# Optimization experiments

Hardware: AMD Instinct MI355X
Metric: run time of the kernel (lower is better)

Reference implementation:

```python
import jax, jax.numpy as jnp
import numpy as np

N = 50000

def gcn_conv(h, W, b, src, dst, n):
    # h: [N, Fin] -> linear transform then normalized scatter-add aggregation
    h = h @ W  # [N, Fout]
    # add self-loops (PyG GCNConv default)
    loop = jnp.arange(n, dtype=src.dtype)
    s = jnp.concatenate([src, loop])
    d = jnp.concatenate([dst, loop])
    # symmetric normalization: deg^{-1/2}[s] * deg^{-1/2}[d], deg over target index
    deg = jax.ops.segment_sum(jnp.ones_like(d, dtype=h.dtype), d, num_segments=n)
    dinv = jnp.where(deg > 0, jax.lax.rsqrt(deg), 0.0)
    norm = dinv[s] * dinv[d]  # [E+N]
    msg = h[s] * norm[:, None]  # gather + scale
    out = jax.ops.segment_sum(msg, d, num_segments=n)  # scatter-add
    return out + b


def setup_inputs() -> dict:
    key = jax.random.key(0)
    k1, k2, k3, k4, k5, k6 = jax.random.split(key, 6)
    Fin, Fh, Fout = 512, 256, 64
    E = 800000
    x = jax.random.normal(k1, (N, Fin), dtype=jnp.float32)
    edge_index = jax.random.randint(k2, (2, E), 0, N, dtype=jnp.int64)
    # Glorot-style init matching nn Parameter scale
    W1 = jax.random.normal(k3, (Fin, Fh), dtype=jnp.float32) * (1.0 / np.sqrt(Fin))
    b1 = jnp.zeros((Fh,), dtype=jnp.float32)
    W2 = jax.random.normal(k4, (Fh, Fout), dtype=jnp.float32) * (1.0 / np.sqrt(Fh))
    b2 = jnp.zeros((Fout,), dtype=jnp.float32)
    return {"x": x, "edge_index": edge_index, "W1": W1, "b1": b1, "W2": W2, "b2": b2}


def reference(x, edge_index, W1, b1, W2, b2):
    src, dst = edge_index[0], edge_index[1]
    h1 = jax.nn.relu(gcn_conv(x, W1, b1, src, dst, N))
    # dropout is identity in eval mode
    h2 = gcn_conv(h1, W2, b2, src, dst, N)
    return jax.nn.log_softmax(h2, axis=1)
```

## Files before the change

### kernel.cpp

```cpp
#include <hip/hip_runtime.h>
#include <hip/hip_bf16.h>

typedef __attribute__((ext_vector_type(8))) short short8;
typedef __attribute__((ext_vector_type(4))) float f32x4;

#define NNODES 50000

__device__ __forceinline__ float b2f(unsigned short s) {
  union { unsigned int u; float f; } c; c.u = ((unsigned int)s) << 16;
  return c.f;
}
__device__ __forceinline__ unsigned short f2b(float f) {
  return __bfloat16_as_ushort(__float2bfloat16(f));
}
__device__ __forceinline__ unsigned int pkcvt(float a, float b) {
  return (unsigned int)f2b(a) | ((unsigned int)f2b(b) << 16);
}

__device__ __forceinline__ void gl_lds16(const void* g, void* l) {
  __builtin_amdgcn_global_load_lds((const __attribute__((address_space(1))) unsigned int*)g,
                                   (__attribute__((address_space(3))) unsigned int*)l, 16, 0, 0);
}

__global__ __launch_bounds__(256) void k_deg(const int* __restrict__ ei, int* __restrict__ deg, int E,
                                             int* __restrict__ rnk,
                                             const float* __restrict__ W1, const float* __restrict__ W2,
                                             unsigned short* __restrict__ w1t, unsigned short* __restrict__ w2t) {
  int idx = blockIdx.x * 256 + threadIdx.x;
  if (idx < E) {
    int r = atomicAdd(&deg[ei[E + idx]], 1);
    rnk[idx] = r;
  }
  if (idx < 256 * 512) { int nn = idx >> 9, kk = idx & 511; w1t[idx] = f2b(W1[kk * 256 + nn]); }
  int i2 = idx - 256 * 512;
  if (i2 >= 0 && i2 < 64 * 256) { int nn = i2 >> 8, kk = i2 & 255; w2t[i2] = f2b(W2[kk * 64 + nn]); }
}

__global__ __launch_bounds__(256) void k_scanA(const int* __restrict__ deg, int* __restrict__ excl,
                                               int* __restrict__ blksum, float* __restrict__ dinv, int n) {
  const int i = blockIdx.x * 256 + threadIdx.x;
  const int lane = threadIdx.x & 63, wid = threadIdx.x >> 6;
  const int v = (i < n) ? deg[i] : 0;
  int x = v;
#pragma unroll
  for (int o = 1; o < 64; o <<= 1) {
    int y = __shfl_up(x, o, 64);
    if (lane >= o) x += y;
  }
  __shared__ int wsum[4];
  if (lane == 63) wsum[wid] = x;
  __syncthreads();
  int woff = 0;
  for (int w = 0; w < wid; ++w) woff += wsum[w];
  const int incl = x + woff;
  if (i < n) {
    excl[i] = incl - v;
    dinv[i] = rsqrtf((float)v + 1.0f);
  }
  if (threadIdx.x == 255) blksum[blockIdx.x] = incl;
}

__global__ __launch_bounds__(256) void k_scanC(const int* __restrict__ excl, const int* __restrict__ blksum,
                                               int* __restrict__ rowptr, int n, int E) {
  const int t = threadIdx.x;
  int partial = 0;
  for (int j = t; j < (int)blockIdx.x; j += 256) partial += blksum[j];
#pragma unroll
  for (int o = 32; o > 0; o >>= 1) partial += __shfl_xor(partial, o, 64);
  __shared__ int ws[4];
  if ((t & 63) == 0) ws[t >> 6] = partial;
  __syncthreads();
  const int off = ws[0] + ws[1] + ws[2] + ws[3];
  const int i = blockIdx.x * 256 + t;
  if (i < n) rowptr[i] = excl[i] + off;
  if (i == 0) rowptr[n] = E;
}

__global__ __launch_bounds__(256) void k_fillx(const int* __restrict__ ei, const int* __restrict__ rowptr,
                                               const int* __restrict__ rnk, int* __restrict__ csr, int E,
                                               const float* __restrict__ x, unsigned short* __restrict__ xb) {
  int idx = blockIdx.x * 256 + threadIdx.x;
  if (idx < E) {
    const int dst = ei[E + idx];
    csr[rowptr[dst] + rnk[idx]] = ei[idx];
  }
  if (idx < (NNODES * 512) / 8) {
    const float4 v0 = *(const float4*)(x + (size_t)idx * 8);
    const float4 v1 = *(const float4*)(x + (size_t)idx * 8 + 4);
    uint4 p;
    p.x = pkcvt(v0.x, v0.y); p.y = pkcvt(v0.z, v0.w);
    p.z = pkcvt(v1.x, v1.y); p.w = pkcvt(v1.z, v1.w);
    *(uint4*)(xb + (size_t)idx * 8) = p;
  }
}

__global__ __launch_bounds__(256) void k_gemm1(const unsigned short* __restrict__ xb,
    const unsigned short* __restrict__ w1t, const float* __restrict__ dinv,
    unsigned short* __restrict__ hs1b) {
  const int M = NNODES, K = 512, N = 256;
  const int NRB = (NNODES + 127) / 128;
  const int bid = blockIdx.x;
  const int rowblk = (bid >> 5) * 8 + (bid & 7);
  const int colblk = (bid >> 3) & 3;
  if (rowblk >= NRB) return;

  __shared__ unsigned short Ab[2][128][32];
  __shared__ unsigned short Bb[2][64][32];

  const int tid = threadIdx.x;
  const int w = tid >> 6, lane = tid & 63;
  const int sub = lane >> 2;
  const int brow = rowblk * 128, bcol = colblk * 64;
  const int wr = w >> 1, wc = w & 1;
  const int lr = lane & 15, lk = lane >> 4;

  const int swc = ((lane & 3) ^ ((lane >> 3) & 3)) * 8;
  const int rch = (lk ^ ((lr >> 1) & 3)) * 8;

  int gr0 = brow + w * 16 + sub;      if (gr0 >= M) gr0 = M - 1;
  int gr1 = brow + 64 + w * 16 + sub; if (gr1 >= M) gr1 = M - 1;
  const int grB = bcol + w * 16 + sub;

  const unsigned short* a0p = xb + (size_t)gr0 * K + swc;
  const unsigned short* a1p = xb + (size_t)gr1 * K + swc;
  const unsigned short* bp  = w1t + (size_t)grB * K + swc;

  f32x4 acc[4][2] = {};

#define G1_STAGE(BUF, KT) do { \
    gl_lds16(a0p + (KT), &Ab[BUF][w * 16][0]); \
    gl_lds16(a1p + (KT), &Ab[BUF][64 + w * 16][0]); \
    gl_lds16(bp  + (KT), &Bb[BUF][w * 16][0]); \
  } while (0)

  G1_STAGE(0, 0);
  G1_STAGE(1, 32);
  asm volatile("s_waitcnt vmcnt(3)" ::: "memory");
  __builtin_amdgcn_s_barrier();

  for (int s = 0; s < 16; ++s) {
    const int cur = s & 1;
    short8 af[4], bf[2];
#pragma unroll
    for (int m = 0; m < 4; ++m) af[m] = *(const short8*)&Ab[cur][wr * 64 + m * 16 + lr][rch];
#pragma unroll
    for (int n = 0; n < 2; ++n) bf[n] = *(const short8*)&Bb[cur][wc * 32 + n * 16 + lr][rch];
    if (s < 14) {
      asm volatile("s_waitcnt lgkmcnt(0)" ::: "memory");
      __builtin_amdgcn_s_barrier();
      G1_STAGE(cur, (s + 2) * 32);
    }
#pragma unroll
    for (int m = 0; m < 4; ++m)
#pragma unroll
      for (int n = 0; n < 2; ++n)
        acc[m][n] = __builtin_amdgcn_mfma_f32_16x16x32_bf16(af[m], bf[n], acc[m][n], 0, 0, 0);
    if (s < 14)      asm volatile("s_waitcnt vmcnt(3)" ::: "memory");
    else if (s == 14) asm volatile("s_waitcnt vmcnt(0)" ::: "memory");
    if (s < 15) __builtin_amdgcn_s_barrier();
  }
#undef G1_STAGE

#pragma unroll
  for (int m = 0; m < 4; ++m) {
#pragma unroll
    for (int n = 0; n < 2; ++n) {
      const int col = bcol + wc * 32 + n * 16 + lr;
#pragma unroll
      for (int j = 0; j < 4; ++j) {
        const int row = brow + wr * 64 + m * 16 + lk * 4 + j;
        if (row < M) hs1b[(size_t)row * N + col] = f2b(acc[m][n][j] * dinv[row]);
      }
    }
  }
}

__global__ __launch_bounds__(256) void k_agg1g(const int* __restrict__ rowptr,
    const int* __restrict__ csr, const unsigned short* __restrict__ hs1b,
    const float* __restrict__ dinv, const float* __restrict__ b1,
    const unsigned short* __restrict__ w2t, unsigned short* __restrict__ hs2b) {
  const int M = NNODES;
  __shared__ unsigned short h1t[16][264];
  const int tid = threadIdx.x;
  const int w = tid >> 6, lane = tid & 63;
  const int lr = lane & 15, lk = lane >> 4;
  const int brow = blockIdx.x * 16;

  const float4 bb = *(const float4*)(b1 + lane * 4);

  for (int i = 0; i < 4; ++i) {
    const int ldsrow = w * 4 + i;
    const int d = brow + ldsrow;
    f32x4 acc = {0.f, 0.f, 0.f, 0.f};
    if (d < M) {
      const int a = rowptr[d], bnd = rowptr[d + 1];
      ushort4 sv = *(const ushort4*)(hs1b + (size_t)d * 256 + lane * 4);
      acc[0] = b2f(sv.x); acc[1] = b2f(sv.y); acc[2] = b2f(sv.z); acc[3] = b2f(sv.w);
      int e = a;
      for (; e + 8 <= bnd; e += 8) {
        int s[8];
#pragma unroll
        for (int j = 0; j < 8; ++j) s[j] = csr[e + j];
        ushort4 v[8];
#pragma unroll
        for (int j = 0; j < 8; ++j) v[j] = *(const ushort4*)(hs1b + (size_t)s[j] * 256 + lane * 4);
#pragma unroll
        for (int j = 0; j < 8; ++j) {
          acc[0] += b2f(v[j].x); acc[1] += b2f(v[j].y);
          acc[2] += b2f(v[j].z); acc[3] += b2f(v[j].w);
        }
      }
      for (; e + 2 <= bnd; e += 2) {
        int s0 = csr[e], s1 = csr[e + 1];
        ushort4 v0 = *(const ushort4*)(hs1b + (size_t)s0 * 256 + lane * 4);
        ushort4 v1 = *(const ushort4*)(hs1b + (size_t)s1 * 256 + lane * 4);
        acc[0] += b2f(v0.x) + b2f(v1.x); acc[1] += b2f(v0.y) + b2f(v1.y);
        acc[2] += b2f(v0.z) + b2f(v1.z); acc[3] += b2f(v0.w) + b2f(v1.w);
      }
      for (; e < bnd; ++e) {
        int s0 = csr[e];
        ushort4 v0 = *(const ushort4*)(hs1b + (size_t)s0 * 256 + lane * 4);
        acc[0] += b2f(v0.x); acc[1] += b2f(v0.y); acc[2] += b2f(v0.z); acc[3] += b2f(v0.w);
      }
      const float di = dinv[d];
      acc[0] = fmaxf(0.f, acc[0] * di + bb.x);
      acc[1] = fmaxf(0.f, acc[1] * di + bb.y);
      acc[2] = fmaxf(0.f, acc[2] * di + bb.z);
      acc[3] = fmaxf(0.f, acc[3] * di + bb.w);
    }
    uint2 pk;
    pk.x = pkcvt(acc[0], acc[1]);
    pk.y = pkcvt(acc[2], acc[3]);
    *(uint2*)&h1t[ldsrow][lane * 4] = pk;
  }

  __syncthreads();

  f32x4 acc2 = {};
#pragma unroll
  for (int s = 0; s < 8; ++s) {
    short8 af = *(const short8*)&h1t[lr][s * 32 + lk * 8];
    short8 bfv = *(const short8*)(w2t + (size_t)(w * 16 + lr) * 256 + s * 32 + lk * 8);
    acc2 = __builtin_amdgcn_mfma_f32_16x16x32_bf16(af, bfv, acc2, 0, 0, 0);
  }

  {
    const int col = w * 16 + lr;
#pragma unroll
    for (int j = 0; j < 4; ++j) {
      const int row = brow + lk * 4 + j;
      if (row < M) hs2b[(size_t)row * 64 + col] = f2b(acc2[j] * dinv[row]);
    }
  }
}

__global__ __launch_bounds__(256) void k_agg2f(const int* __restrict__ rowptr,
    const int* __restrict__ csr, const unsigned short* __restrict__ hs2b,
    const float* __restrict__ dinv, const float* __restrict__ b2,
    float* __restrict__ out) {
  const int d = blockIdx.x * 4 + (threadIdx.x >> 6);
  if (d >= NNODES) return;
  const int lane = threadIdx.x & 63;
  const int a = rowptr[d], bnd = rowptr[d + 1];

  float acc = b2f(hs2b[(size_t)d * 64 + lane]);

  int i = a;
  for (; i + 16 <= bnd; i += 16) {
    int s[16];
#pragma unroll
    for (int j = 0; j < 16; ++j) s[j] = csr[i + j];
    unsigned short v[16];
#pragma unroll
    for (int j = 0; j < 16; ++j) v[j] = hs2b[(size_t)s[j] * 64 + lane];
#pragma unroll
    for (int j = 0; j < 16; ++j) acc += b2f(v[j]);
  }
  for (; i + 4 <= bnd; i += 4) {
    int s[4];
#pragma unroll
    for (int j = 0; j < 4; ++j) s[j] = csr[i + j];
    unsigned short v[4];
#pragma unroll
    for (int j = 0; j < 4; ++j) v[j] = hs2b[(size_t)s[j] * 64 + lane];
#pragma unroll
    for (int j = 0; j < 4; ++j) acc += b2f(v[j]);
  }
  for (; i < bnd; ++i) acc += b2f(hs2b[(size_t)csr[i] * 64 + lane]);

  float v = acc * dinv[d] + b2[lane];
  float m = v;
#pragma unroll
  for (int o = 32; o > 0; o >>= 1) m = fmaxf(m, __shfl_xor(m, o, 64));
  float ex = expf(v - m);
  float s = ex;
#pragma unroll
  for (int o = 32; o > 0; o >>= 1) s += __shfl_xor(s, o, 64);
  out[(size_t)d * 64 + lane] = v - m - logf(s);
}

extern "C" void kernel_launch(void* const* d_in, const int* in_sizes, int n_in,
                              void* d_out, int out_size, void* d_ws, size_t ws_size,
                              hipStream_t stream) {
  const float* x  = (const float*)d_in[0];
  const int*   ei = (const int*)d_in[1];
  const float* W1 = (const float*)d_in[2];
  const float* b1 = (const float*)d_in[3];
  const float* W2 = (const float*)d_in[4];
  const float* b2 = (const float*)d_in[5];
  float* out = (float*)d_out;
  const int E = in_sizes[1] / 2;
  const int n = NNODES;
  const int nblk = (n + 255) / 256;

  char* ws = (char*)d_ws;
  size_t off = 0;
  auto alloc = [&](size_t bytes) { char* p = ws + off; off = (off + bytes + 255) & ~(size_t)255; return p; };
  int*            deg    = (int*)alloc((size_t)n * 4);
  float*          dinv   = (float*)alloc((size_t)n * 4);
  int*            excl   = (int*)alloc((size_t)n * 4);
  int*            blksum = (int*)alloc((size_t)nblk * 4);
  int*            rowptr = (int*)alloc((size_t)(n + 1) * 4);
  int*            rnk    = (int*)alloc((size_t)E * 4);
  int*            csr    = (int*)alloc((size_t)E * 4);
  unsigned short* w1t    = (unsigned short*)alloc(256 * 512 * 2);
  unsigned short* w2t    = (unsigned short*)alloc(64 * 256 * 2);
  unsigned short* hs1b   = (unsigned short*)alloc((size_t)n * 256 * 2);
  unsigned short* hs2b   = (unsigned short*)alloc((size_t)n * 64 * 2);
  unsigned short* xb     = (unsigned short*)alloc((size_t)n * 512 * 2);
  (void)ws_size; (void)n_in; (void)out_size;

  hipMemsetAsync(deg, 0, (size_t)n * 4, stream);
  k_deg<<<(E + 255) / 256, 256, 0, stream>>>(ei, deg, E, rnk, W1, W2, w1t, w2t);
  k_scanA<<<nblk, 256, 0, stream>>>(deg, excl, blksum, dinv, n);
  k_scanC<<<nblk, 256, 0, stream>>>(excl, blksum, rowptr, n, E);
  k_fillx<<<(NNODES * 512 / 8 + 255) / 256, 256, 0, stream>>>(ei, rowptr, rnk, csr, E, x, xb);
  k_gemm1<<<49 * 32, 256, 0, stream>>>(xb, w1t, dinv, hs1b);
  k_agg1g<<<(n + 15) / 16, 256, 0, stream>>>(rowptr, csr, hs1b, dinv, b1, w2t, hs2b);
  k_agg2f<<<(n + 3) / 4, 256, 0, stream>>>(rowptr, csr, hs2b, dinv, b2, out);
}
```

Before: 218.6 us.

## Split layer-1 features into column halves and unfuse aggregation from second GEMM

GEMM1 now writes its output as two 128-column planes, so each aggregation block gathers 256-byte rows from a 12.8 MB plane instead of 512-byte rows from the full matrix. Blocks alternate between halves, which is meant to improve cache locality for the random gathers. The layer-2 GEMM moves out of the aggregation kernel into a separate pipelined MFMA kernel that reads the aggregated plane through LDS. This adds an extra 25.6 MB intermediate written and read back, plus one more launch.

```diff
diff --git a/kernel.cpp b/kernel.cpp
--- a/kernel.cpp
+++ b/kernel.cpp
@@ -96,8 +96,8 @@
 
 __global__ __launch_bounds__(256) void k_gemm1(const unsigned short* __restrict__ xb,
     const unsigned short* __restrict__ w1t, const float* __restrict__ dinv,
-    unsigned short* __restrict__ hs1b) {
-  const int M = NNODES, K = 512, N = 256;
+    unsigned short* __restrict__ hs1h) {
+  const int M = NNODES, K = 512;
   const int NRB = (NNODES + 127) / 128;
   const int bid = blockIdx.x;
   const int rowblk = (bid >> 5) * 8 + (bid & 7);
@@ -166,90 +166,137 @@
 #pragma unroll
     for (int n = 0; n < 2; ++n) {
       const int col = bcol + wc * 32 + n * 16 + lr;
+      unsigned short* dsth = hs1h + (size_t)(col >> 7) * ((size_t)NNODES * 128);
+      const int cw = col & 127;
 #pragma unroll
       for (int j = 0; j < 4; ++j) {
         const int row = brow + wr * 64 + m * 16 + lk * 4 + j;
-        if (row < M) hs1b[(size_t)row * N + col] = f2b(acc[m][n][j] * dinv[row]);
+        if (row < M) dsth[(size_t)row * 128 + cw] = f2b(acc[m][n][j] * dinv[row]);
       }
     }
   }
 }
 
-__global__ __launch_bounds__(256) void k_agg1g(const int* __restrict__ rowptr,
-    const int* __restrict__ csr, const unsigned short* __restrict__ hs1b,
+__global__ __launch_bounds__(256) void k_agg1(const int* __restrict__ rowptr,
+    const int* __restrict__ csr, const unsigned short* __restrict__ hs1h,
     const float* __restrict__ dinv, const float* __restrict__ b1,
-    const unsigned short* __restrict__ w2t, unsigned short* __restrict__ hs2b) {
+    unsigned short* __restrict__ h1agg) {
+  const int half = blockIdx.x & 1;
+  const int chunk = blockIdx.x >> 1;
+  const int w = threadIdx.x >> 6, lane = threadIdx.x & 63;
+  const int d = chunk * 4 + w;
+  if (d >= NNODES) return;
+  const unsigned short* __restrict__ src = hs1h + (size_t)half * ((size_t)NNODES * 128);
+  const int a = rowptr[d], bnd = rowptr[d + 1];
+
+  unsigned int sv = *(const unsigned int*)(src + (size_t)d * 128 + lane * 2);
+  float a0 = b2f((unsigned short)(sv & 0xffff));
+  float a1 = b2f((unsigned short)(sv >> 16));
+
+  int e = a;
+  for (; e + 8 <= bnd; e += 8) {
+    int s[8];
+#pragma unroll
+    for (int j = 0; j < 8; ++j) s[j] = csr[e + j];
+    unsigned int v[8];
+#pragma unroll
+    for (int j = 0; j < 8; ++j) v[j] = *(const unsigned int*)(src + (size_t)s[j] * 128 + lane * 2);
+#pragma unroll
+    for (int j = 0; j < 8; ++j) {
+      a0 += b2f((unsigned short)(v[j] & 0xffff));
+      a1 += b2f((unsigned short)(v[j] >> 16));
+    }
+  }
+  for (; e + 2 <= bnd; e += 2) {
+    int s0 = csr[e], s1 = csr[e + 1];
+    unsigned int v0 = *(const unsigned int*)(src + (size_t)s0 * 128 + lane * 2);
+    unsigned int v1 = *(const unsigned int*)(src + (size_t)s1 * 128 + lane * 2);
+    a0 += b2f((unsigned short)(v0 & 0xffff)) + b2f((unsigned short)(v1 & 0xffff));
+    a1 += b2f((unsigned short)(v0 >> 16)) + b2f((unsigned short)(v1 >> 16));
+  }
+  for (; e < bnd; ++e) {
+    int s0 = csr[e];
+    unsigned int v0 = *(const unsigned int*)(src + (size_t)s0 * 128 + lane * 2);
+    a0 += b2f((unsigned short)(v0 & 0xffff));
+    a1 += b2f((unsigned short)(v0 >> 16));
+  }
+
+  const float di = dinv[d];
+  const float2 bb = *(const float2*)(b1 + half * 128 + lane * 2);
+  a0 = fmaxf(0.f, a0 * di + bb.x);
+  a1 = fmaxf(0.f, a1 * di + bb.y);
+  *(unsigned int*)(h1agg + (size_t)half * ((size_t)NNODES * 128) + (size_t)d * 128 + lane * 2) =
+      pkcvt(a0, a1);
+}
+
+__global__ __launch_bounds__(256) void k_gemm2(const unsigned short* __restrict__ h1agg,
+    const unsigned short* __restrict__ w2t, const float* __restrict__ dinv,
+    unsigned short* __restrict__ hs2b) {
   const int M = NNODES;
-  __shared__ unsigned short h1t[16][264];
+  const size_t HL = (size_t)NNODES * 128;
+  const int brow = blockIdx.x * 64;
+
+  __shared__ unsigned short As[2][64][32];
+  __shared__ unsigned short Bs[2][64][32];
+
   const int tid = threadIdx.x;
   const int w = tid >> 6, lane = tid & 63;
+  const int sub = lane >> 2;
+  const int wr = w >> 1, wc = w & 1;
   const int lr = lane & 15, lk = lane >> 4;
-  const int brow = blockIdx.x * 16;
-
-  const float4 bb = *(const float4*)(b1 + lane * 4);
-
-  for (int i = 0; i < 4; ++i) {
-    const int ldsrow = w * 4 + i;
-    const int d = brow + ldsrow;
-    f32x4 acc = {0.f, 0.f, 0.f, 0.f};
-    if (d < M) {
-      const int a = rowptr[d], bnd = rowptr[d + 1];
-      ushort4 sv = *(const ushort4*)(hs1b + (size_t)d * 256 + lane * 4);
-      acc[0] = b2f(sv.x); acc[1] = b2f(sv.y); acc[2] = b2f(sv.z); acc[3] = b2f(sv.w);
-      int e = a;
-      for (; e + 8 <= bnd; e += 8) {
-        int s[8];
-#pragma unroll
-        for (int j = 0; j < 8; ++j) s[j] = csr[e + j];
-        ushort4 v[8];
-#pragma unroll
-        for (int j = 0; j < 8; ++j) v[j] = *(const ushort4*)(hs1b + (size_t)s[j] * 256 + lane * 4);
-#pragma unroll
-        for (int j = 0; j < 8; ++j) {
-          acc[0] += b2f(v[j].x); acc[1] += b2f(v[j].y);
-          acc[2] += b2f(v[j].z); acc[3] += b2f(v[j].w);
-        }
+
+  const int swc = ((lane & 3) ^ ((lane >> 3) & 3)) * 8;
+  const int rch = (lk ^ ((lr >> 1) & 3)) * 8;
+
+  int gr = brow + w * 16 + sub; if (gr >= M) gr = M - 1;
+  const unsigned short* ap = h1agg + (size_t)gr * 128 + swc;
+  const unsigned short* bp = w2t + (size_t)(w * 16 + sub) * 256 + swc;
+
+  f32x4 acc[2][2] = {};
+
+#define G2_STAGE(BUF, S) do { \
+    gl_lds16(ap + (size_t)((S) >> 2) * HL + ((S) & 3) * 32, &As[BUF][w * 16][0]); \
+    gl_lds16(bp + (S) * 32,                                  &Bs[BUF][w * 16][0]); \
+  } while (0)
+
+  G2_STAGE(0, 0);
+  G2_STAGE(1, 1);
+  asm volatile("s_waitcnt vmcnt(2)" ::: "memory");
+  __builtin_amdgcn_s_barrier();
+
+  for (int s = 0; s < 8; ++s) {
+    const int cur = s & 1;
+    short8 af[2], bf[2];
+#pragma unroll
+    for (int m = 0; m < 2; ++m) af[m] = *(const short8*)&As[cur][wr * 32 + m * 16 + lr][rch];
+#pragma unroll
+    for (int n = 0; n < 2; ++n) bf[n] = *(const short8*)&Bs[cur][wc * 32 + n * 16 + lr][rch];
+    if (s < 6) {
+      asm volatile("s_waitcnt lgkmcnt(0)" ::: "memory");
+      __builtin_amdgcn_s_barrier();
+      G2_STAGE(cur, s + 2);
+    }
+#pragma unroll
+    for (int m = 0; m < 2; ++m)
+#pragma unroll
+      for (int n = 0; n < 2; ++n)
+        acc[m][n] = __builtin_amdgcn_mfma_f32_16x16x32_bf16(af[m], bf[n], acc[m][n], 0, 0, 0);
+    if (s < 6)      asm volatile("s_waitcnt vmcnt(2)" ::: "memory");
+    else if (s == 6) asm volatile("s_waitcnt vmcnt(0)" ::: "memory");
+    if (s < 7) __builtin_amdgcn_s_barrier();
+  }
+#undef G2_STAGE
+
+#pragma unroll
+  for (int m = 0; m < 2; ++m) {
+#pragma unroll
+    for (int n = 0; n < 2; ++n) {
+      const int col = wc * 32 + n * 16 + lr;
+#pragma unroll
+      for (int j = 0; j < 4; ++j) {
+        const int row = brow + wr * 32 + m * 16 + lk * 4 + j;
+        if (row < M) hs2b[(size_t)row * 64 + col] = f2b(acc[m][n][j] * dinv[row]);
       }
-      for (; e + 2 <= bnd; e += 2) {
-        int s0 = csr[e], s1 = csr[e + 1];
-        ushort4 v0 = *(const ushort4*)(hs1b + (size_t)s0 * 256 + lane * 4);
-        ushort4 v1 = *(const ushort4*)(hs1b + (size_t)s1 * 256 + lane * 4);
-        acc[0] += b2f(v0.x) + b2f(v1.x); acc[1] += b2f(v0.y) + b2f(v1.y);
-        acc[2] += b2f(v0.z) + b2f(v1.z); acc[3] += b2f(v0.w) + b2f(v1.w);
-      }
-      for (; e < bnd; ++e) {
-        int s0 = csr[e];
-        ushort4 v0 = *(const ushort4*)(hs1b + (size_t)s0 * 256 + lane * 4);
-        acc[0] += b2f(v0.x); acc[1] += b2f(v0.y); acc[2] += b2f(v0.z); acc[3] += b2f(v0.w);
-      }
-      const float di = dinv[d];
-      acc[0] = fmaxf(0.f, acc[0] * di + bb.x);
-      acc[1] = fmaxf(0.f, acc[1] * di + bb.y);
-      acc[2] = fmaxf(0.f, acc[2] * di + bb.z);
-      acc[3] = fmaxf(0.f, acc[3] * di + bb.w);
-    }
-    uint2 pk;
-    pk.x = pkcvt(acc[0], acc[1]);
-    pk.y = pkcvt(acc[2], acc[3]);
-    *(uint2*)&h1t[ldsrow][lane * 4] = pk;
-  }
-
-  __syncthreads();
-
-  f32x4 acc2 = {};
-#pragma unroll
-  for (int s = 0; s < 8; ++s) {
-    short8 af = *(const short8*)&h1t[lr][s * 32 + lk * 8];
-    short8 bfv = *(const short8*)(w2t + (size_t)(w * 16 + lr) * 256 + s * 32 + lk * 8);
-    acc2 = __builtin_amdgcn_mfma_f32_16x16x32_bf16(af, bfv, acc2, 0, 0, 0);
-  }
-
-  {
-    const int col = w * 16 + lr;
-#pragma unroll
-    for (int j = 0; j < 4; ++j) {
-      const int row = brow + lk * 4 + j;
-      if (row < M) hs2b[(size_t)row * 64 + col] = f2b(acc2[j] * dinv[row]);
     }
   }
 }
@@ -325,7 +372,8 @@
   int*            csr    = (int*)alloc((size_t)E * 4);
   unsigned short* w1t    = (unsigned short*)alloc(256 * 512 * 2);
   unsigned short* w2t    = (unsigned short*)alloc(64 * 256 * 2);
-  unsigned short* hs1b   = (unsigned short*)alloc((size_t)n * 256 * 2);
+  unsigned short* hs1h   = (unsigned short*)alloc((size_t)n * 256 * 2);
+  unsigned short* h1agg  = (unsigned short*)alloc((size_t)n * 256 * 2);
   unsigned short* hs2b   = (unsigned short*)alloc((size_t)n * 64 * 2);
   unsigned short* xb     = (unsigned short*)alloc((size_t)n * 512 * 2);
   (void)ws_size; (void)n_in; (void)out_size;
@@ -335,7 +383,8 @@
   k_scanA<<<nblk, 256, 0, stream>>>(deg, excl, blksum, dinv, n);
   k_scanC<<<nblk, 256, 0, stream>>>(excl, blksum, rowptr, n, E);
   k_fillx<<<(NNODES * 512 / 8 + 255) / 256, 256, 0, stream>>>(ei, rowptr, rnk, csr, E, x, xb);
-  k_gemm1<<<49 * 32, 256, 0, stream>>>(xb, w1t, dinv, hs1b);
-  k_agg1g<<<(n + 15) / 16, 256, 0, stream>>>(rowptr, csr, hs1b, dinv, b1, w2t, hs2b);
+  k_gemm1<<<49 * 32, 256, 0, stream>>>(xb, w1t, dinv, hs1h);
+  k_agg1<<<12500 * 2, 256, 0, stream>>>(rowptr, csr, hs1h, dinv, b1, h1agg);
+  k_gemm2<<<(n + 63) / 64, 256, 0, stream>>>(h1agg, w2t, dinv, hs2b);
   k_agg2f<<<(n + 3) / 4, 256, 0, stream>>>(rowptr, csr, hs2b, dinv, b2, out);
 }
```

Result: no change. 220.6 us (+0.9%).
